# Performance work log

Hardware: AMD Instinct MI355X
Metric: run time of the kernel (lower is better)

Reference implementation:

```python
import jax, jax.numpy as jnp
import numpy as np

B, T, H = 64, 1024, 1024


def setup_inputs() -> dict:
    key = jax.random.key(0)
    ks = jax.random.split(key, 8)
    s = 1.0 / np.sqrt(H)
    return {
        "spatial_feats": jax.random.normal(ks[0], (B, T, H), dtype=jnp.float32),
        "hidden_state": jax.random.normal(ks[1], (B, H), dtype=jnp.float32),
        "W_enc": jax.random.uniform(ks[2], (H, H), jnp.float32, -s, s),
        "b_enc": jax.random.uniform(ks[3], (H,), jnp.float32, -s, s),
        "W_dec": jax.random.uniform(ks[4], (H, H), jnp.float32, -s, s),
        "b_dec": jax.random.uniform(ks[5], (H,), jnp.float32, -s, s),
        "w_score": jax.random.uniform(ks[6], (H,), jnp.float32, -s, s),
        "b_score": jax.random.uniform(ks[7], (), jnp.float32, -s, s),
    }


def reference(spatial_feats, hidden_state, W_enc, b_enc, W_dec, b_dec, w_score, b_score):
    # decoder_proj(hidden_state): [B, H] -> [B, 1, H]
    dec = (jnp.einsum("bh,oh->bo", hidden_state, W_dec) + b_dec)[:, None, :]
    # encoder_proj(spatial_feats): [B, T, H]
    enc = jnp.einsum("bth,oh->bto", spatial_feats, W_enc) + b_enc
    energy = jnp.tanh(enc + dec)                      # [B, T, H]
    scores = jnp.einsum("bth,h->bt", energy, w_score) + b_score  # [B, T]
    weights = jax.nn.softmax(scores, axis=1)          # [B, T]
    context = jnp.einsum("bth,bt->bh", spatial_feats, weights)   # [B, H]
    return (context, weights)
```

## Files before the change

### kernel.cpp

```cpp
#include <hip/hip_runtime.h>
#include <hip/hip_bf16.h>
#include <math.h>


typedef __attribute__((ext_vector_type(8))) short bf16x8;
typedef __attribute__((ext_vector_type(8))) unsigned short ushort8;
typedef __attribute__((ext_vector_type(4))) float f32x4;

__device__ __forceinline__ unsigned short f2bf(float f) {
  union { float f; unsigned int u; } v; v.f = f;
  unsigned int r = v.u + 0x7FFFu + ((v.u >> 16) & 1u);
  return (unsigned short)(r >> 16);
}

__device__ __forceinline__ void gld16(const void* g, void* l) {
  __builtin_amdgcn_global_load_lds(
      (const __attribute__((address_space(1))) void*)g,
      (__attribute__((address_space(3))) void*)l, 16, 0, 0);
}

__global__ void cvt_bf16_kernel(const float* __restrict__ src,
                                unsigned short* __restrict__ dst, int n8) {
  int i = blockIdx.x * blockDim.x + threadIdx.x;
  if (i >= n8) return;
  const float4* s4 = (const float4*)src;
  float4 a = s4[(size_t)i * 2], b = s4[(size_t)i * 2 + 1];
  ushort8 o;
  o[0] = f2bf(a.x); o[1] = f2bf(a.y); o[2] = f2bf(a.z); o[3] = f2bf(a.w);
  o[4] = f2bf(b.x); o[5] = f2bf(b.y); o[6] = f2bf(b.z); o[7] = f2bf(b.w);
  *(ushort8*)(dst + (size_t)i * 8) = o;
}

__global__ void dec_kernel(const float* __restrict__ hidden,
                           const float* __restrict__ W_dec,
                           const float* __restrict__ b_dec,
                           float* __restrict__ dec) {
  int wave = threadIdx.x >> 6, lane = threadIdx.x & 63;
  int o = (blockIdx.x >> 2) * 4 + wave;
  int kc = (blockIdx.x & 3) * 256;
  const float4* hid4 = (const float4*)(hidden + (size_t)lane * 1024 + kc);
  const float4* w4   = (const float4*)(W_dec + (size_t)o * 1024 + kc);
  float4 acc; acc.x = acc.y = acc.z = acc.w = 0.f;
  #pragma unroll 4
  for (int i = 0; i < 64; i++) {
    float4 x = hid4[i], y = w4[i];
    acc.x = fmaf(x.x, y.x, acc.x);
    acc.y = fmaf(x.y, y.y, acc.y);
    acc.z = fmaf(x.z, y.z, acc.z);
    acc.w = fmaf(x.w, y.w, acc.w);
  }
  float v = (acc.x + acc.y) + (acc.z + acc.w);
  if ((blockIdx.x & 3) == 0) v += b_dec[o];
  atomicAdd(&dec[lane * 1024 + o], v);
}

__global__ __launch_bounds__(256) void enc_score_bf16_kernel(
    const unsigned short* __restrict__ A,
    const unsigned short* __restrict__ W,
    const float* __restrict__ b_enc,
    const float* __restrict__ dec,
    const float* __restrict__ w_score,
    float* __restrict__ scores)
{
  __shared__ unsigned short As[128 * 32];
  __shared__ unsigned short Bs[128 * 32];

  const int bid = blockIdx.x;
  const int n0 = (bid & 7) * 128;
  const int m0 = (bid >> 3) * 128;
  const int tid = threadIdx.x;
  const int lane = tid & 63, wave = tid >> 6;
  const int wm = (wave >> 1) * 64, wn = (wave & 1) * 64;
  const int quad = lane >> 4, col = lane & 15;

  const int srow = wave * 32 + (lane >> 2);
  const int scol = (lane & 3) * 8;
  const unsigned short* ga = A + (size_t)(m0 + srow) * 1024 + scol;
  const unsigned short* gb = W + (size_t)(n0 + srow) * 1024 + scol;
  unsigned short* la = As + wave * 32 * 32;
  unsigned short* lb = Bs + wave * 32 * 32;

  f32x4 acc[4][4];
  #pragma unroll
  for (int mi = 0; mi < 4; mi++)
    #pragma unroll
    for (int ni = 0; ni < 4; ni++)
      acc[mi][ni] = (f32x4){0.f, 0.f, 0.f, 0.f};

  for (int k0 = 0; k0 < 1024; k0 += 32) {
    gld16(ga + k0,             la);
    gld16(ga + k0 + 16 * 1024, la + 16 * 32);
    gld16(gb + k0,             lb);
    gld16(gb + k0 + 16 * 1024, lb + 16 * 32);
    __syncthreads();
    bf16x8 af[4], bfr[4];
    #pragma unroll
    for (int i = 0; i < 4; i++) {
      af[i]  = *(const bf16x8*)(As + (wm + i * 16 + col) * 32 + quad * 8);
      bfr[i] = *(const bf16x8*)(Bs + (wn + i * 16 + col) * 32 + quad * 8);
    }
    #pragma unroll
    for (int mi = 0; mi < 4; mi++)
      #pragma unroll
      for (int ni = 0; ni < 4; ni++)
        acc[mi][ni] = __builtin_amdgcn_mfma_f32_16x16x32_bf16(
            af[mi], bfr[ni], acc[mi][ni], 0, 0, 0);
    __syncthreads();
  }

  const int b = m0 >> 10;
  float decv[4], wsv[4];
  #pragma unroll
  for (int ni = 0; ni < 4; ni++) {
    int n = n0 + wn + ni * 16 + col;
    decv[ni] = dec[b * 1024 + n] + b_enc[n];
    wsv[ni] = w_score[n];
  }
  #pragma unroll
  for (int mi = 0; mi < 4; mi++) {
    float rs[4] = {0.f, 0.f, 0.f, 0.f};
    #pragma unroll
    for (int ni = 0; ni < 4; ni++)
      #pragma unroll
      for (int r = 0; r < 4; r++)
        rs[r] += tanhf(acc[mi][ni][r] + decv[ni]) * wsv[ni];
    #pragma unroll
    for (int r = 0; r < 4; r++) {
      float v = rs[r];
      v += __shfl_xor(v, 1);
      v += __shfl_xor(v, 2);
      v += __shfl_xor(v, 4);
      v += __shfl_xor(v, 8);
      if (col == 0)
        atomicAdd(&scores[m0 + wm + mi * 16 + quad * 4 + r], v);
    }
  }
}

__global__ __launch_bounds__(256) void enc_score_f32_kernel(
    const float* __restrict__ A, const float* __restrict__ W,
    const float* __restrict__ b_enc, const float* __restrict__ dec,
    const float* __restrict__ w_score, float* __restrict__ scores) {
  __shared__ unsigned short As[128][32];
  __shared__ unsigned short Bs[128][32];
  const int bid = blockIdx.x;
  const int n0 = (bid & 7) * 128;
  const int m0 = (bid >> 3) * 128;
  const int tid = threadIdx.x;
  const int lane = tid & 63, wave = tid >> 6;
  const int wm = (wave >> 1) * 64, wn = (wave & 1) * 64;
  const int quad = lane >> 4, col = lane & 15;
  const int srow = tid >> 3;
  const int scol = (tid & 7) * 4;
  f32x4 acc[4][4];
  #pragma unroll
  for (int mi = 0; mi < 4; mi++)
    #pragma unroll
    for (int ni = 0; ni < 4; ni++)
      acc[mi][ni] = (f32x4){0.f, 0.f, 0.f, 0.f};
  for (int k0 = 0; k0 < 1024; k0 += 32) {
    #pragma unroll
    for (int p = 0; p < 4; p++) {
      int r = p * 32 + srow;
      float4 va = *(const float4*)(A + (size_t)(m0 + r) * 1024 + (k0 + scol));
      float4 vb = *(const float4*)(W + (size_t)(n0 + r) * 1024 + (k0 + scol));
      ushort4 pa, pb;
      pa.x = f2bf(va.x); pa.y = f2bf(va.y); pa.z = f2bf(va.z); pa.w = f2bf(va.w);
      pb.x = f2bf(vb.x); pb.y = f2bf(vb.y); pb.z = f2bf(vb.z); pb.w = f2bf(vb.w);
      *(ushort4*)(&As[r][scol]) = pa;
      *(ushort4*)(&Bs[r][scol]) = pb;
    }
    __syncthreads();
    bf16x8 af[4], bfr[4];
    #pragma unroll
    for (int i = 0; i < 4; i++) {
      af[i]  = *(const bf16x8*)(&As[wm + i * 16 + col][quad * 8]);
      bfr[i] = *(const bf16x8*)(&Bs[wn + i * 16 + col][quad * 8]);
    }
    #pragma unroll
    for (int mi = 0; mi < 4; mi++)
      #pragma unroll
      for (int ni = 0; ni < 4; ni++)
        acc[mi][ni] = __builtin_amdgcn_mfma_f32_16x16x32_bf16(
            af[mi], bfr[ni], acc[mi][ni], 0, 0, 0);
    __syncthreads();
  }
  const int b = m0 >> 10;
  float decv[4], wsv[4];
  #pragma unroll
  for (int ni = 0; ni < 4; ni++) {
    int n = n0 + wn + ni * 16 + col;
    decv[ni] = dec[b * 1024 + n] + b_enc[n];
    wsv[ni] = w_score[n];
  }
  #pragma unroll
  for (int mi = 0; mi < 4; mi++) {
    float rs[4] = {0.f, 0.f, 0.f, 0.f};
    #pragma unroll
    for (int ni = 0; ni < 4; ni++)
      #pragma unroll
      for (int r = 0; r < 4; r++)
        rs[r] += tanhf(acc[mi][ni][r] + decv[ni]) * wsv[ni];
    #pragma unroll
    for (int r = 0; r < 4; r++) {
      float v = rs[r];
      v += __shfl_xor(v, 1);
      v += __shfl_xor(v, 2);
      v += __shfl_xor(v, 4);
      v += __shfl_xor(v, 8);
      if (col == 0)
        atomicAdd(&scores[m0 + wm + mi * 16 + quad * 4 + r], v);
    }
  }
}

__global__ void softmax_kernel(const float* __restrict__ scores,
                               float* __restrict__ weights) {
  __shared__ float red[256];
  int b = blockIdx.x, tid = threadIdx.x;
  const float* s = scores + b * 1024;
  float v[4];
  float mx = -1e30f;
  #pragma unroll
  for (int i = 0; i < 4; i++) { v[i] = s[tid + i * 256]; mx = fmaxf(mx, v[i]); }
  red[tid] = mx; __syncthreads();
  for (int off = 128; off > 0; off >>= 1) {
    if (tid < off) red[tid] = fmaxf(red[tid], red[tid + off]);
    __syncthreads();
  }
  mx = red[0]; __syncthreads();
  float sum = 0.f;
  #pragma unroll
  for (int i = 0; i < 4; i++) { v[i] = __expf(v[i] - mx); sum += v[i]; }
  red[tid] = sum; __syncthreads();
  for (int off = 128; off > 0; off >>= 1) {
    if (tid < off) red[tid] += red[tid + off];
    __syncthreads();
  }
  float inv = 1.0f / red[0];
  #pragma unroll
  for (int i = 0; i < 4; i++) weights[b * 1024 + tid + i * 256] = v[i] * inv;
}

__global__ void context_kernel(const float* __restrict__ spatial,
                               const float* __restrict__ weights,
                               float* __restrict__ context) {
  int b = blockIdx.x >> 3, tq = blockIdx.x & 7;
  int tid = threadIdx.x;
  __shared__ float wl[128];
  if (tid < 128) wl[tid] = weights[b * 1024 + tq * 128 + tid];
  __syncthreads();
  const float4* sp =
      (const float4*)(spatial + ((size_t)(b * 1024 + tq * 128)) * 1024);
  float4 acc; acc.x = acc.y = acc.z = acc.w = 0.f;
  #pragma unroll 4
  for (int t = 0; t < 128; t++) {
    float w = wl[t];
    float4 x = sp[(size_t)t * 256 + tid];
    acc.x = fmaf(w, x.x, acc.x);
    acc.y = fmaf(w, x.y, acc.y);
    acc.z = fmaf(w, x.z, acc.z);
    acc.w = fmaf(w, x.w, acc.w);
  }
  float* c = context + b * 1024 + tid * 4;
  atomicAdd(c + 0, acc.x);
  atomicAdd(c + 1, acc.y);
  atomicAdd(c + 2, acc.z);
  atomicAdd(c + 3, acc.w);
}

extern "C" void kernel_launch(void* const* d_in, const int* in_sizes, int n_in,
                              void* d_out, int out_size, void* d_ws, size_t ws_size,
                              hipStream_t stream) {
  const float* spatial  = (const float*)d_in[0];
  const float* hidden   = (const float*)d_in[1];
  const float* W_enc    = (const float*)d_in[2];
  const float* b_enc    = (const float*)d_in[3];
  const float* W_dec    = (const float*)d_in[4];
  const float* b_dec    = (const float*)d_in[5];
  const float* w_score  = (const float*)d_in[6];

  float* out      = (float*)d_out;
  float* context  = out;
  float* weights  = out + 65536;

  float* scores   = (float*)d_ws;
  float* dec      = scores + 65536;
  unsigned short* Wbf = (unsigned short*)(dec + 65536);
  unsigned short* Abf = Wbf + 1024 * 1024;

  const size_t need = 512 * 1024 + 2ull * 1024 * 1024 + 2ull * 65536 * 1024;

  hipMemsetAsync(scores, 0, 2 * 65536 * sizeof(float), stream);
  hipMemsetAsync(context, 0, 65536 * sizeof(float), stream);

  dec_kernel<<<1024, 256, 0, stream>>>(hidden, W_dec, b_dec, dec);

  if (ws_size >= need) {
    cvt_bf16_kernel<<<512, 256, 0, stream>>>(W_enc, Wbf, 1024 * 1024 / 8);
    cvt_bf16_kernel<<<32768, 256, 0, stream>>>(spatial, Abf, 65536 * 1024 / 8);
    enc_score_bf16_kernel<<<4096, 256, 0, stream>>>(Abf, Wbf, b_enc, dec,
                                                    w_score, scores);
  } else {
    enc_score_f32_kernel<<<4096, 256, 0, stream>>>(spatial, W_enc, b_enc, dec,
                                                   w_score, scores);
  }

  softmax_kernel<<<64, 256, 0, stream>>>(scores, weights);
  context_kernel<<<512, 256, 0, stream>>>(spatial, weights, context);
}
```

Measured before the change: 702.9 us.

## Fuse prep work into one kernel, unroll K-loop by 64, use fast tanh

Merges the two bf16 conversion kernels, the decoder projection and the score zeroing into a single prep kernel. The decoder projection is now computed per batch row from shared memory without atomics, and b_enc is folded into dec. The memsets are removed and context is zeroed inside the softmax kernel. The GEMM now loads 64 K-elements per barrier pair using two LDS buffers, which halves the number of syncs, and tanhf is replaced with an exp-based approximation. The cost is a larger prep grid, more LDS per block, and a small loss of tanh accuracy.

```diff
diff --git a/kernel.cpp b/kernel.cpp
--- a/kernel.cpp
+++ b/kernel.cpp
@@ -4,7 +4,6 @@
 
 
 typedef __attribute__((ext_vector_type(8))) short bf16x8;
-typedef __attribute__((ext_vector_type(8))) unsigned short ushort8;
 typedef __attribute__((ext_vector_type(4))) float f32x4;
 
 __device__ __forceinline__ unsigned short f2bf(float f) {
@@ -13,57 +12,71 @@
   return (unsigned short)(r >> 16);
 }
 
+__device__ __forceinline__ float fast_tanh(float x) {
+  float e = __expf(2.0f * x);
+  return 1.0f - 2.0f / (e + 1.0f);
+}
+
 __device__ __forceinline__ void gld16(const void* g, void* l) {
   __builtin_amdgcn_global_load_lds(
       (const __attribute__((address_space(1))) void*)g,
       (__attribute__((address_space(3))) void*)l, 16, 0, 0);
 }
 
-__global__ void cvt_bf16_kernel(const float* __restrict__ src,
-                                unsigned short* __restrict__ dst, int n8) {
-  int i = blockIdx.x * blockDim.x + threadIdx.x;
-  if (i >= n8) return;
-  const float4* s4 = (const float4*)src;
-  float4 a = s4[(size_t)i * 2], b = s4[(size_t)i * 2 + 1];
-  ushort8 o;
-  o[0] = f2bf(a.x); o[1] = f2bf(a.y); o[2] = f2bf(a.z); o[3] = f2bf(a.w);
-  o[4] = f2bf(b.x); o[5] = f2bf(b.y); o[6] = f2bf(b.z); o[7] = f2bf(b.w);
-  *(ushort8*)(dst + (size_t)i * 8) = o;
-}
-
-__global__ void dec_kernel(const float* __restrict__ hidden,
-                           const float* __restrict__ W_dec,
-                           const float* __restrict__ b_dec,
-                           float* __restrict__ dec) {
-  int wave = threadIdx.x >> 6, lane = threadIdx.x & 63;
-  int o = (blockIdx.x >> 2) * 4 + wave;
-  int kc = (blockIdx.x & 3) * 256;
-  const float4* hid4 = (const float4*)(hidden + (size_t)lane * 1024 + kc);
-  const float4* w4   = (const float4*)(W_dec + (size_t)o * 1024 + kc);
-  float4 acc; acc.x = acc.y = acc.z = acc.w = 0.f;
-  #pragma unroll 4
-  for (int i = 0; i < 64; i++) {
-    float4 x = hid4[i], y = w4[i];
-    acc.x = fmaf(x.x, y.x, acc.x);
-    acc.y = fmaf(x.y, y.y, acc.y);
-    acc.z = fmaf(x.z, y.z, acc.z);
-    acc.w = fmaf(x.w, y.w, acc.w);
-  }
-  float v = (acc.x + acc.y) + (acc.z + acc.w);
-  if ((blockIdx.x & 3) == 0) v += b_dec[o];
-  atomicAdd(&dec[lane * 1024 + o], v);
+__global__ __launch_bounds__(256) void prep_kernel(
+    const float* __restrict__ spatial, const float* __restrict__ hidden,
+    const float* __restrict__ W_enc, const float* __restrict__ b_enc,
+    const float* __restrict__ W_dec, const float* __restrict__ b_dec,
+    unsigned short* __restrict__ Wbf, unsigned short* __restrict__ Abf,
+    float* __restrict__ dec, float* __restrict__ scores, int nW, int nA) {
+  __shared__ float hs[1024];
+  const int bid = blockIdx.x, tid = threadIdx.x;
+  if (bid < nW + nA) {
+    const float* src = (bid < nW) ? W_enc : spatial;
+    unsigned short* dst = (bid < nW) ? Wbf : Abf;
+    size_t g4 = (size_t)(bid < nW ? bid : bid - nW) * 256 + tid;
+    float4 v = ((const float4*)src)[g4];
+    ushort4 o;
+    o.x = f2bf(v.x); o.y = f2bf(v.y); o.z = f2bf(v.z); o.w = f2bf(v.w);
+    *(ushort4*)(dst + g4 * 4) = o;
+    return;
+  }
+  const int dbid = bid - nW - nA;
+  const int b = dbid >> 3, o0 = (dbid & 7) * 128;
+  const int wave = tid >> 6, lane = tid & 63;
+  int gid = dbid * 256 + tid;
+  if (gid < 65536) scores[gid] = 0.f;
+  ((float4*)hs)[tid] = ((const float4*)(hidden + (size_t)b * 1024))[tid];
+  __syncthreads();
+  for (int it = 0; it < 32; it++) {
+    int o = o0 + it * 4 + wave;
+    const float4* w4 = (const float4*)(W_dec + (size_t)o * 1024);
+    float4 acc; acc.x = acc.y = acc.z = acc.w = 0.f;
+    #pragma unroll
+    for (int j = 0; j < 4; j++) {
+      int i = j * 64 + lane;
+      float4 x = ((const float4*)hs)[i], y = w4[i];
+      acc.x = fmaf(x.x, y.x, acc.x);
+      acc.y = fmaf(x.y, y.y, acc.y);
+      acc.z = fmaf(x.z, y.z, acc.z);
+      acc.w = fmaf(x.w, y.w, acc.w);
+    }
+    float v = (acc.x + acc.y) + (acc.z + acc.w);
+    #pragma unroll
+    for (int off = 1; off < 64; off <<= 1) v += __shfl_xor(v, off);
+    if (lane == 0) dec[b * 1024 + o] = v + b_dec[o] + b_enc[o];
+  }
 }
 
 __global__ __launch_bounds__(256) void enc_score_bf16_kernel(
     const unsigned short* __restrict__ A,
     const unsigned short* __restrict__ W,
-    const float* __restrict__ b_enc,
     const float* __restrict__ dec,
     const float* __restrict__ w_score,
     float* __restrict__ scores)
 {
-  __shared__ unsigned short As[128 * 32];
-  __shared__ unsigned short Bs[128 * 32];
+  __shared__ unsigned short As[2][128 * 32];
+  __shared__ unsigned short Bs[2][128 * 32];
 
   const int bid = blockIdx.x;
   const int n0 = (bid & 7) * 128;
@@ -71,14 +84,13 @@
   const int tid = threadIdx.x;
   const int lane = tid & 63, wave = tid >> 6;
   const int wm = (wave >> 1) * 64, wn = (wave & 1) * 64;
-  const int quad = lane >> 4, col = lane & 15;
+  const int quad = lane >> 4, colL = lane & 15;
 
   const int srow = wave * 32 + (lane >> 2);
   const int scol = (lane & 3) * 8;
   const unsigned short* ga = A + (size_t)(m0 + srow) * 1024 + scol;
   const unsigned short* gb = W + (size_t)(n0 + srow) * 1024 + scol;
-  unsigned short* la = As + wave * 32 * 32;
-  unsigned short* lb = Bs + wave * 32 * 32;
+  const int lbase0 = wave * 32 * 32 + lane * 8;
 
   f32x4 acc[4][4];
   #pragma unroll
@@ -87,24 +99,33 @@
     for (int ni = 0; ni < 4; ni++)
       acc[mi][ni] = (f32x4){0.f, 0.f, 0.f, 0.f};
 
-  for (int k0 = 0; k0 < 1024; k0 += 32) {
-    gld16(ga + k0,             la);
-    gld16(ga + k0 + 16 * 1024, la + 16 * 32);
-    gld16(gb + k0,             lb);
-    gld16(gb + k0 + 16 * 1024, lb + 16 * 32);
-    __syncthreads();
-    bf16x8 af[4], bfr[4];
-    #pragma unroll
-    for (int i = 0; i < 4; i++) {
-      af[i]  = *(const bf16x8*)(As + (wm + i * 16 + col) * 32 + quad * 8);
-      bfr[i] = *(const bf16x8*)(Bs + (wn + i * 16 + col) * 32 + quad * 8);
-    }
-    #pragma unroll
-    for (int mi = 0; mi < 4; mi++)
-      #pragma unroll
-      for (int ni = 0; ni < 4; ni++)
-        acc[mi][ni] = __builtin_amdgcn_mfma_f32_16x16x32_bf16(
-            af[mi], bfr[ni], acc[mi][ni], 0, 0, 0);
+  for (int k0 = 0; k0 < 1024; k0 += 64) {
+    #pragma unroll
+    for (int kh = 0; kh < 2; kh++) {
+      #pragma unroll
+      for (int j = 0; j < 2; j++) {
+        int goff = k0 + kh * 32 + j * 16 * 1024;
+        int loff = lbase0 + j * 16 * 32;
+        gld16(ga + goff, &As[kh][loff]);
+        gld16(gb + goff, &Bs[kh][loff]);
+      }
+    }
+    __syncthreads();
+    #pragma unroll
+    for (int kh = 0; kh < 2; kh++) {
+      bf16x8 af[4], bfr[4];
+      #pragma unroll
+      for (int i = 0; i < 4; i++) {
+        af[i]  = *(const bf16x8*)(&As[kh][(wm + i * 16 + colL) * 32 + quad * 8]);
+        bfr[i] = *(const bf16x8*)(&Bs[kh][(wn + i * 16 + colL) * 32 + quad * 8]);
+      }
+      #pragma unroll
+      for (int mi = 0; mi < 4; mi++)
+        #pragma unroll
+        for (int ni = 0; ni < 4; ni++)
+          acc[mi][ni] = __builtin_amdgcn_mfma_f32_16x16x32_bf16(
+              af[mi], bfr[ni], acc[mi][ni], 0, 0, 0);
+    }
     __syncthreads();
   }
 
@@ -112,8 +133,8 @@
   float decv[4], wsv[4];
   #pragma unroll
   for (int ni = 0; ni < 4; ni++) {
-    int n = n0 + wn + ni * 16 + col;
-    decv[ni] = dec[b * 1024 + n] + b_enc[n];
+    int n = n0 + wn + ni * 16 + colL;
+    decv[ni] = dec[b * 1024 + n];
     wsv[ni] = w_score[n];
   }
   #pragma unroll
@@ -123,7 +144,7 @@
     for (int ni = 0; ni < 4; ni++)
       #pragma unroll
       for (int r = 0; r < 4; r++)
-        rs[r] += tanhf(acc[mi][ni][r] + decv[ni]) * wsv[ni];
+        rs[r] += fast_tanh(acc[mi][ni][r] + decv[ni]) * wsv[ni];
     #pragma unroll
     for (int r = 0; r < 4; r++) {
       float v = rs[r];
@@ -131,7 +152,7 @@
       v += __shfl_xor(v, 2);
       v += __shfl_xor(v, 4);
       v += __shfl_xor(v, 8);
-      if (col == 0)
+      if (colL == 0)
         atomicAdd(&scores[m0 + wm + mi * 16 + quad * 4 + r], v);
     }
   }
@@ -139,8 +160,8 @@
 
 __global__ __launch_bounds__(256) void enc_score_f32_kernel(
     const float* __restrict__ A, const float* __restrict__ W,
-    const float* __restrict__ b_enc, const float* __restrict__ dec,
-    const float* __restrict__ w_score, float* __restrict__ scores) {
+    const float* __restrict__ dec, const float* __restrict__ w_score,
+    float* __restrict__ scores) {
   __shared__ unsigned short As[128][32];
   __shared__ unsigned short Bs[128][32];
   const int bid = blockIdx.x;
@@ -149,7 +170,7 @@
   const int tid = threadIdx.x;
   const int lane = tid & 63, wave = tid >> 6;
   const int wm = (wave >> 1) * 64, wn = (wave & 1) * 64;
-  const int quad = lane >> 4, col = lane & 15;
+  const int quad = lane >> 4, colL = lane & 15;
   const int srow = tid >> 3;
   const int scol = (tid & 7) * 4;
   f32x4 acc[4][4];
@@ -174,8 +195,8 @@
     bf16x8 af[4], bfr[4];
     #pragma unroll
     for (int i = 0; i < 4; i++) {
-      af[i]  = *(const bf16x8*)(&As[wm + i * 16 + col][quad * 8]);
-      bfr[i] = *(const bf16x8*)(&Bs[wn + i * 16 + col][quad * 8]);
+      af[i]  = *(const bf16x8*)(&As[wm + i * 16 + colL][quad * 8]);
+      bfr[i] = *(const bf16x8*)(&Bs[wn + i * 16 + colL][quad * 8]);
     }
     #pragma unroll
     for (int mi = 0; mi < 4; mi++)
@@ -189,8 +210,8 @@
   float decv[4], wsv[4];
   #pragma unroll
   for (int ni = 0; ni < 4; ni++) {
-    int n = n0 + wn + ni * 16 + col;
-    decv[ni] = dec[b * 1024 + n] + b_enc[n];
+    int n = n0 + wn + ni * 16 + colL;
+    decv[ni] = dec[b * 1024 + n];
     wsv[ni] = w_score[n];
   }
   #pragma unroll
@@ -200,7 +221,7 @@
     for (int ni = 0; ni < 4; ni++)
       #pragma unroll
       for (int r = 0; r < 4; r++)
-        rs[r] += tanhf(acc[mi][ni][r] + decv[ni]) * wsv[ni];
+        rs[r] += fast_tanh(acc[mi][ni][r] + decv[ni]) * wsv[ni];
     #pragma unroll
     for (int r = 0; r < 4; r++) {
       float v = rs[r];
@@ -208,16 +229,19 @@
       v += __shfl_xor(v, 2);
       v += __shfl_xor(v, 4);
       v += __shfl_xor(v, 8);
-      if (col == 0)
+      if (colL == 0)
         atomicAdd(&scores[m0 + wm + mi * 16 + quad * 4 + r], v);
     }
   }
 }
 
 __global__ void softmax_kernel(const float* __restrict__ scores,
-                               float* __restrict__ weights) {
+                               float* __restrict__ weights,
+                               float* __restrict__ context) {
   __shared__ float red[256];
   int b = blockIdx.x, tid = threadIdx.x;
+  float4 z; z.x = z.y = z.z = z.w = 0.f;
+  ((float4*)context)[blockIdx.x * 256 + tid] = z;
   const float* s = scores + b * 1024;
   float v[4];
   float mx = -1e30f;
@@ -291,21 +315,21 @@
 
   const size_t need = 512 * 1024 + 2ull * 1024 * 1024 + 2ull * 65536 * 1024;
 
-  hipMemsetAsync(scores, 0, 2 * 65536 * sizeof(float), stream);
-  hipMemsetAsync(context, 0, 65536 * sizeof(float), stream);
-
-  dec_kernel<<<1024, 256, 0, stream>>>(hidden, W_dec, b_dec, dec);
-
   if (ws_size >= need) {
-    cvt_bf16_kernel<<<512, 256, 0, stream>>>(W_enc, Wbf, 1024 * 1024 / 8);
-    cvt_bf16_kernel<<<32768, 256, 0, stream>>>(spatial, Abf, 65536 * 1024 / 8);
-    enc_score_bf16_kernel<<<4096, 256, 0, stream>>>(Abf, Wbf, b_enc, dec,
-                                                    w_score, scores);
+    const int nW = 1024, nA = 65536;
+    prep_kernel<<<nW + nA + 512, 256, 0, stream>>>(
+        spatial, hidden, W_enc, b_enc, W_dec, b_dec, Wbf, Abf, dec, scores,
+        nW, nA);
+    enc_score_bf16_kernel<<<4096, 256, 0, stream>>>(Abf, Wbf, dec, w_score,
+                                                    scores);
   } else {
-    enc_score_f32_kernel<<<4096, 256, 0, stream>>>(spatial, W_enc, b_enc, dec,
+    prep_kernel<<<512, 256, 0, stream>>>(
+        spatial, hidden, W_enc, b_enc, W_dec, b_dec, nullptr, nullptr, dec,
+        scores, 0, 0);
+    enc_score_f32_kernel<<<4096, 256, 0, stream>>>(spatial, W_enc, dec,
                                                    w_score, scores);
   }
 
-  softmax_kernel<<<64, 256, 0, stream>>>(scores, weights);
+  softmax_kernel<<<64, 256, 0, stream>>>(scores, weights, context);
   context_kernel<<<512, 256, 0, stream>>>(spatial, weights, context);
 }
```

After: 688.3 us. -2.1%, faster.
